# Kernel optimization log

Measured on AMD Instinct MI355X. Metric: run time of the kernel, lower is better.

The kernel has to match this reference:

```python
import jax, jax.numpy as jnp
import numpy as np

FILTER_K = 100  # filter_K from __init__
NUM_CLASSES = 1000


def setup_inputs() -> dict:
    key = jax.random.key(0)
    ks = jax.random.split(key, 7)
    B, Din, D, C, N = 256, 2048, 512, NUM_CLASSES, 50000
    x = jax.random.normal(ks[0], (B, Din), jnp.float32)
    Wf = jax.random.normal(ks[1], (Din, D), jnp.float32) * 0.02
    Wc = jax.random.normal(ks[2], (C, D), jnp.float32) * 0.05
    bc = jax.random.normal(ks[3], (C,), jnp.float32) * 0.01
    supports_in = jax.random.normal(ks[4], (N, D), jnp.float32)
    ent_in = jax.random.uniform(ks[5], (N,), jnp.float32)
    labels_idx = jax.random.randint(ks[6], (N,), 0, C)
    return {"x": x, "Wf": Wf, "Wc": Wc, "bc": bc,
            "supports_in": supports_in, "ent_in": ent_in, "labels_idx": labels_idx}


def _softmax_entropy(logits):
    # -(softmax * log_softmax).sum(1), computed stably in one pass
    logp = jax.nn.log_softmax(logits, axis=1)
    return -(jnp.exp(logp) * logp).sum(axis=1)


def reference(x, Wf, Wc, bc, supports_in, ent_in, labels_idx):
    C = Wc.shape[0]
    z = x @ Wf                    # featurizer: [B, D]
    p = z @ Wc.T + bc             # classifier logits: [B, C]
    yhat = jax.nn.one_hot(jnp.argmax(p, axis=1), C, dtype=z.dtype)
    ent_new = _softmax_entropy(p)
    labels_in = jax.nn.one_hot(labels_idx, C, dtype=z.dtype)

    # grow support memory
    supports = jnp.concatenate([supports_in, z], axis=0)   # [M, D]
    labels = jnp.concatenate([labels_in, yhat], axis=0)    # [M, C]
    ent = jnp.concatenate([ent_in, ent_new], axis=0)       # [M]

    # select_supports: per-class keep FILTER_K lowest-entropy entries.
    # Torch gathers a variable-size subset; equivalent fixed-shape form is a
    # boolean mask (non-selected rows contribute zero to the weights matmul).
    y = jnp.argmax(labels, axis=1)
    M = ent.shape[0]
    order = jnp.lexsort((ent, y))            # sort by class, then entropy
    y_sorted = y[order]
    # rank of each entry within its class segment
    rank = jnp.arange(M) - jnp.searchsorted(y_sorted, y_sorted, side='left')
    mask = jnp.zeros((M,), bool).at[order].set(rank < FILTER_K)
    maskf = mask.astype(z.dtype)

    # normalize supports row-wise (F.normalize, eps=1e-12), then masked matmul
    s_norm = supports / jnp.maximum(
        jnp.linalg.norm(supports, axis=1, keepdims=True), 1e-12)
    weights = (s_norm * maskf[:, None]).T @ (labels * maskf[:, None])  # [D, C]
    weights = weights / jnp.maximum(
        jnp.linalg.norm(weights, axis=0, keepdims=True), 1e-12)
    return z @ weights            # [B, C]
```

## Files before the change

kernel.cpp:

```cpp
#include <hip/hip_runtime.h>
#include <hip/hip_bf16.h>
#include <math.h>

#define BB   256
#define DIN  2048
#define DD   512
#define CC   1000
#define NN   50000
#define MM   (NN + BB)
#define FILTER_K 100
#define SLOT 512

#define SK1  32
#define SKP  8

#define Z_OFF     0
#define CNT_OFF   (Z_OFF + BB*DD)
#define ENTS_OFF  (CNT_OFF + 1024)
#define IDXS_OFF  (ENTS_OFF + CC*SLOT)
#define WN_OFF    (IDXS_OFF + CC*SLOT)
#define ZP_OFF    (WN_OFF + CC*DD)
#define PP_OFF    (ZP_OFF + SK1*BB*DD)
#define OP_OFF    (PP_OFF + SKP*BB*CC)

__global__ __launch_bounds__(256, 2) void gemm_ab_part(
    const float* __restrict__ A, const float* __restrict__ B,
    float* __restrict__ Cp) {
  __shared__ float As[16][68];
  __shared__ float Bs[16][132];
  const int tid = threadIdx.x;
  const int m0 = blockIdx.y * 64;
  const int n0 = blockIdx.x * 128;
  const int k0 = blockIdx.z * 64;
  const int ar = tid >> 2, ac = (tid & 3) * 4;
  const int br = tid >> 4, bcn = (tid & 15) * 8;
  const int tm = (tid >> 4) * 4, tn = (tid & 15) * 4;
  float acc[4][8] = {};
  float4 av  = *(const float4*)&A[(size_t)(m0 + ar) * DIN + k0 + ac];
  float4 bv0 = *(const float4*)&B[(size_t)(k0 + br) * DD + n0 + bcn];
  float4 bv1 = *(const float4*)&B[(size_t)(k0 + br) * DD + n0 + bcn + 4];
  for (int kk = 0; kk < 64; kk += 16) {
    __syncthreads();
    As[ac + 0][ar] = av.x; As[ac + 1][ar] = av.y;
    As[ac + 2][ar] = av.z; As[ac + 3][ar] = av.w;
    *(float4*)&Bs[br][bcn] = bv0;
    *(float4*)&Bs[br][bcn + 4] = bv1;
    __syncthreads();
    if (kk + 16 < 64) {
      av  = *(const float4*)&A[(size_t)(m0 + ar) * DIN + k0 + kk + 16 + ac];
      bv0 = *(const float4*)&B[(size_t)(k0 + kk + 16 + br) * DD + n0 + bcn];
      bv1 = *(const float4*)&B[(size_t)(k0 + kk + 16 + br) * DD + n0 + bcn + 4];
    }
#pragma unroll
    for (int q = 0; q < 16; ++q) {
      float4 a  = *(const float4*)&As[q][tm];
      float4 b0 = *(const float4*)&Bs[q][tn];
      float4 b1 = *(const float4*)&Bs[q][tn + 64];
      float aa[4] = {a.x, a.y, a.z, a.w};
      float bb[8] = {b0.x, b0.y, b0.z, b0.w, b1.x, b1.y, b1.z, b1.w};
#pragma unroll
      for (int i = 0; i < 4; ++i)
#pragma unroll
        for (int j = 0; j < 8; ++j) acc[i][j] += aa[i] * bb[j];
    }
  }
  float* Cb = Cp + (size_t)blockIdx.z * BB * DD;
#pragma unroll
  for (int i = 0; i < 4; ++i) {
    *(float4*)&Cb[(size_t)(m0 + tm + i) * DD + n0 + tn] =
        make_float4(acc[i][0], acc[i][1], acc[i][2], acc[i][3]);
    *(float4*)&Cb[(size_t)(m0 + tm + i) * DD + n0 + 64 + tn] =
        make_float4(acc[i][4], acc[i][5], acc[i][6], acc[i][7]);
  }
}

__global__ __launch_bounds__(256, 2) void gemm_abt_part(
    const float* __restrict__ A, const float* __restrict__ Bm,
    float* __restrict__ Cp) {
  __shared__ float As[16][68];
  __shared__ float Bs[16][68];
  const int tid = threadIdx.x;
  const int m0 = blockIdx.y * 64;
  const int n0 = blockIdx.x * 64;
  const int k0 = blockIdx.z * 64;
  const int ar = tid >> 2, ac = (tid & 3) * 4;
  const int tm = (tid >> 4) * 4, tn = (tid & 15) * 4;
  float acc[4][4] = {};
  float4 av = *(const float4*)&A[(size_t)(m0 + ar) * DD + k0 + ac];
  float4 bv = make_float4(0.f, 0.f, 0.f, 0.f);
  if (n0 + ar < CC) bv = *(const float4*)&Bm[(size_t)(n0 + ar) * DD + k0 + ac];
  for (int kk = 0; kk < 64; kk += 16) {
    __syncthreads();
    As[ac + 0][ar] = av.x; As[ac + 1][ar] = av.y;
    As[ac + 2][ar] = av.z; As[ac + 3][ar] = av.w;
    Bs[ac + 0][ar] = bv.x; Bs[ac + 1][ar] = bv.y;
    Bs[ac + 2][ar] = bv.z; Bs[ac + 3][ar] = bv.w;
    __syncthreads();
    if (kk + 16 < 64) {
      av = *(const float4*)&A[(size_t)(m0 + ar) * DD + k0 + kk + 16 + ac];
      if (n0 + ar < CC)
        bv = *(const float4*)&Bm[(size_t)(n0 + ar) * DD + k0 + kk + 16 + ac];
    }
#pragma unroll
    for (int q = 0; q < 16; ++q) {
      float4 a = *(const float4*)&As[q][tm];
      float4 b = *(const float4*)&Bs[q][tn];
      float aa[4] = {a.x, a.y, a.z, a.w};
      float bb[4] = {b.x, b.y, b.z, b.w};
#pragma unroll
      for (int i = 0; i < 4; ++i)
#pragma unroll
        for (int j = 0; j < 4; ++j) acc[i][j] += aa[i] * bb[j];
    }
  }
  float* Cb = Cp + (size_t)blockIdx.z * BB * CC;
#pragma unroll
  for (int i = 0; i < 4; ++i) {
    int n = n0 + tn;
    if (n + 3 < CC) {
      *(float4*)&Cb[(size_t)(m0 + tm + i) * CC + n] =
          make_float4(acc[i][0], acc[i][1], acc[i][2], acc[i][3]);
    } else {
#pragma unroll
      for (int j = 0; j < 4; ++j)
        if (n + j < CC) Cb[(size_t)(m0 + tm + i) * CC + n + j] = acc[i][j];
    }
  }
}

template <int S>
__global__ __launch_bounds__(256) void reduce_part(
    const float* __restrict__ part, float* __restrict__ out, int n4) {
  int i = blockIdx.x * 256 + threadIdx.x;
  if (i >= n4) return;
  const float4* p4 = (const float4*)part;
  float4 a = p4[i];
#pragma unroll
  for (int s = 1; s < S; ++s) {
    float4 b = p4[(size_t)s * n4 + i];
    a.x += b.x; a.y += b.y; a.z += b.z; a.w += b.w;
  }
  ((float4*)out)[i] = a;
}

__global__ void scatter_old(const int* __restrict__ labels_idx,
                            const float* __restrict__ ent_in,
                            int* __restrict__ cnt,
                            float* __restrict__ ent_s, int* __restrict__ idx_s) {
  int m = blockIdx.x * blockDim.x + threadIdx.x;
  if (m >= NN) return;
  int c = labels_idx[m];
  int pos = atomicAdd(&cnt[c], 1);
  if (pos < SLOT) {
    ent_s[(size_t)c * SLOT + pos] = ent_in[m];
    idx_s[(size_t)c * SLOT + pos] = m;
  }
}

__global__ __launch_bounds__(256) void rowstats(
    const float* __restrict__ ppart, const float* __restrict__ bc,
    int* __restrict__ cnt, float* __restrict__ ent_s,
    int* __restrict__ idx_s) {
  const int b = blockIdx.x, tid = threadIdx.x;
  const int lane = tid & 63, wid = tid >> 6;
  float r[4];
  float mv = -INFINITY; int mi = 0x7fffffff;
#pragma unroll
  for (int i = 0; i < 4; ++i) {
    int c = tid + 256 * i;
    if (c < CC) {
      float v = bc[c];
#pragma unroll
      for (int s = 0; s < SKP; ++s)
        v += ppart[(size_t)s * BB * CC + (size_t)b * CC + c];
      r[i] = v;
    } else r[i] = -INFINITY;
    if (r[i] > mv) { mv = r[i]; mi = c; }
  }
#pragma unroll
  for (int o = 32; o > 0; o >>= 1) {
    float ov = __shfl_down(mv, o, 64);
    int oi = __shfl_down(mi, o, 64);
    if (ov > mv || (ov == mv && oi < mi)) { mv = ov; mi = oi; }
  }
  __shared__ float smv[4]; __shared__ int smi[4];
  __shared__ float ssm[4], tsm[4];
  if (lane == 0) { smv[wid] = mv; smi[wid] = mi; }
  __syncthreads();
  if (tid == 0) {
#pragma unroll
    for (int w = 1; w < 4; ++w)
      if (smv[w] > smv[0] || (smv[w] == smv[0] && smi[w] < smi[0])) {
        smv[0] = smv[w]; smi[0] = smi[w];
      }
  }
  __syncthreads();
  const float m = smv[0]; const int am = smi[0];
  float s = 0.f, t = 0.f;
#pragma unroll
  for (int i = 0; i < 4; ++i) {
    if (tid + 256 * i < CC) {
      float u = r[i] - m;
      float e = expf(u);
      s += e; t += u * e;
    }
  }
#pragma unroll
  for (int o = 32; o > 0; o >>= 1) {
    s += __shfl_down(s, o, 64);
    t += __shfl_down(t, o, 64);
  }
  if (lane == 0) { ssm[wid] = s; tsm[wid] = t; }
  __syncthreads();
  if (tid == 0) {
    float S = ssm[0] + ssm[1] + ssm[2] + ssm[3];
    float T = tsm[0] + tsm[1] + tsm[2] + tsm[3];
    float ent = logf(S) - T / S;
    int pos = atomicAdd(&cnt[am], 1);
    if (pos < SLOT) {
      ent_s[(size_t)am * SLOT + pos] = ent;
      idx_s[(size_t)am * SLOT + pos] = NN + b;
    }
  }
}

__global__ __launch_bounds__(256) void class_weights(
    const float* __restrict__ supports_in, const float* __restrict__ z,
    const float* __restrict__ ent_s, const int* __restrict__ idx_s,
    const int* __restrict__ cnt, float* __restrict__ wn) {
  const int c = blockIdx.x, tid = threadIdx.x;
  const int lane = tid & 63, wid = tid >> 6;
  int n = cnt[c]; if (n > SLOT) n = SLOT;

  __shared__ int sel[SLOT];
  __shared__ float se[SLOT];
  __shared__ int si[SLOT];
  int seln;
  if (n <= FILTER_K) {
    seln = n;
    for (int i = tid; i < n; i += 256) sel[i] = idx_s[(size_t)c * SLOT + i];
  } else {
    for (int i = tid; i < SLOT; i += 256) {
      if (i < n) { se[i] = ent_s[(size_t)c * SLOT + i]; si[i] = idx_s[(size_t)c * SLOT + i]; }
      else       { se[i] = INFINITY;                     si[i] = 0x7fffffff; }
    }
    __syncthreads();
    for (int k = 2; k <= SLOT; k <<= 1)
      for (int j = k >> 1; j > 0; j >>= 1) {
        for (int i = tid; i < SLOT; i += 256) {
          int ixj = i ^ j;
          if (ixj > i) {
            bool up = ((i & k) == 0);
            float e1 = se[i], e2 = se[ixj];
            int i1 = si[i], i2 = si[ixj];
            bool gt = (e1 > e2) || (e1 == e2 && i1 > i2);
            if (gt == up) { se[i] = e2; se[ixj] = e1; si[i] = i2; si[ixj] = i1; }
          }
        }
        __syncthreads();
      }
    seln = FILTER_K;
    for (int i = tid; i < FILTER_K; i += 256) sel[i] = si[i];
  }
  __syncthreads();

  float4 a0 = make_float4(0.f, 0.f, 0.f, 0.f), a1 = a0;
  const int npair = seln >> 1;
  for (int t = wid; t < npair; t += 4) {
    int r0 = sel[2 * t], r1 = sel[2 * t + 1];
    const float4* p0 = (const float4*)((r0 < NN)
        ? supports_in + (size_t)r0 * DD : z + (size_t)(r0 - NN) * DD);
    const float4* p1 = (const float4*)((r1 < NN)
        ? supports_in + (size_t)r1 * DD : z + (size_t)(r1 - NN) * DD);
    float4 u0 = p0[lane * 2], u1 = p0[lane * 2 + 1];
    float4 w0 = p1[lane * 2], w1 = p1[lane * 2 + 1];
    float s0 = u0.x * u0.x + u0.y * u0.y + u0.z * u0.z + u0.w * u0.w
             + u1.x * u1.x + u1.y * u1.y + u1.z * u1.z + u1.w * u1.w;
    float s1 = w0.x * w0.x + w0.y * w0.y + w0.z * w0.z + w0.w * w0.w
             + w1.x * w1.x + w1.y * w1.y + w1.z * w1.z + w1.w * w1.w;
#pragma unroll
    for (int o = 1; o < 64; o <<= 1) {
      s0 += __shfl_xor(s0, o, 64);
      s1 += __shfl_xor(s1, o, 64);
    }
    float c0 = 1.0f / fmaxf(sqrtf(s0), 1e-12f);
    float c1 = 1.0f / fmaxf(sqrtf(s1), 1e-12f);
    a0.x += u0.x * c0 + w0.x * c1; a0.y += u0.y * c0 + w0.y * c1;
    a0.z += u0.z * c0 + w0.z * c1; a0.w += u0.w * c0 + w0.w * c1;
    a1.x += u1.x * c0 + w1.x * c1; a1.y += u1.y * c0 + w1.y * c1;
    a1.z += u1.z * c0 + w1.z * c1; a1.w += u1.w * c0 + w1.w * c1;
  }
  if ((seln & 1) && wid == (npair & 3)) {
    int r0 = sel[seln - 1];
    const float4* p0 = (const float4*)((r0 < NN)
        ? supports_in + (size_t)r0 * DD : z + (size_t)(r0 - NN) * DD);
    float4 u0 = p0[lane * 2], u1 = p0[lane * 2 + 1];
    float s0 = u0.x * u0.x + u0.y * u0.y + u0.z * u0.z + u0.w * u0.w
             + u1.x * u1.x + u1.y * u1.y + u1.z * u1.z + u1.w * u1.w;
#pragma unroll
    for (int o = 1; o < 64; o <<= 1) s0 += __shfl_xor(s0, o, 64);
    float c0 = 1.0f / fmaxf(sqrtf(s0), 1e-12f);
    a0.x += u0.x * c0; a0.y += u0.y * c0; a0.z += u0.z * c0; a0.w += u0.w * c0;
    a1.x += u1.x * c0; a1.y += u1.y * c0; a1.z += u1.z * c0; a1.w += u1.w * c0;
  }

  __shared__ float part[4][DD];
  *(float4*)&part[wid][lane * 8] = a0;
  *(float4*)&part[wid][lane * 8 + 4] = a1;
  __syncthreads();
  const int d = tid * 2;
  float wx = part[0][d] + part[1][d] + part[2][d] + part[3][d];
  float wy = part[0][d + 1] + part[1][d + 1] + part[2][d + 1] + part[3][d + 1];
  float ss = wx * wx + wy * wy;
#pragma unroll
  for (int o = 1; o < 64; o <<= 1) ss += __shfl_xor(ss, o, 64);
  __shared__ float tot[4];
  if (lane == 0) tot[wid] = ss;
  __syncthreads();
  float S = tot[0] + tot[1] + tot[2] + tot[3];
  float sc = 1.0f / fmaxf(sqrtf(S), 1e-12f);
  ((float2*)(wn + (size_t)c * DD))[tid] = make_float2(wx * sc, wy * sc);
}

extern "C" void kernel_launch(void* const* d_in, const int* in_sizes, int n_in,
                              void* d_out, int out_size, void* d_ws, size_t ws_size,
                              hipStream_t stream) {
  (void)in_sizes; (void)n_in; (void)out_size; (void)ws_size;
  const float* x           = (const float*)d_in[0];
  const float* Wf          = (const float*)d_in[1];
  const float* Wc          = (const float*)d_in[2];
  const float* bc          = (const float*)d_in[3];
  const float* supports_in = (const float*)d_in[4];
  const float* ent_in      = (const float*)d_in[5];
  const int*   labels_idx  = (const int*)d_in[6];
  float* out = (float*)d_out;

  float* W = (float*)d_ws;
  float* z     = W + Z_OFF;
  int*   cnt   = (int*)(W + CNT_OFF);
  float* ent_s = W + ENTS_OFF;
  int*   idx_s = (int*)(W + IDXS_OFF);
  float* wn    = W + WN_OFF;
  float* zpart = W + ZP_OFF;
  float* ppart = W + PP_OFF;
  float* opart = W + OP_OFF;

  hipMemsetAsync(cnt, 0, 1024 * sizeof(int), stream);

  scatter_old<<<(NN + 255) / 256, 256, 0, stream>>>(
      labels_idx, ent_in, cnt, ent_s, idx_s);

  gemm_ab_part<<<dim3(DD / 128, BB / 64, SK1), 256, 0, stream>>>(x, Wf, zpart);
  reduce_part<SK1><<<(BB * DD / 4 + 255) / 256, 256, 0, stream>>>(
      zpart, z, BB * DD / 4);

  gemm_abt_part<<<dim3((CC + 63) / 64, BB / 64, SKP), 256, 0, stream>>>(
      z, Wc, ppart);
  rowstats<<<BB, 256, 0, stream>>>(ppart, bc, cnt, ent_s, idx_s);

  class_weights<<<CC, 256, 0, stream>>>(supports_in, z, ent_s, idx_s, cnt, wn);

  gemm_abt_part<<<dim3((CC + 63) / 64, BB / 64, SKP), 256, 0, stream>>>(
      z, wn, opart);
  reduce_part<SKP><<<(BB * CC / 4 + 255) / 256, 256, 0, stream>>>(
      opart, out, BB * CC / 4);
}
```

Before: 225.9 us.

## Fuse scatter into first GEMM, batch support loads, replace split-K output GEMM

The label scatter is folded into the first GEMM launch as extra blocks past index 512, which removes one kernel launch and lets the scatter run alongside the GEMM. In class_weights, each wavefront now loads four support rows at once, padding the selection list to a multiple of 16 so more memory requests are in flight. The final z·wn product drops split-K and its reduction kernel in favour of a single full-K GEMM with 32x64 tiles. That removes the partial-sum buffer traffic and one launch, but each block now runs a longer serial K loop.

```diff
diff --git a/kernel.cpp b/kernel.cpp
--- a/kernel.cpp
+++ b/kernel.cpp
@@ -21,17 +21,31 @@
 #define WN_OFF    (IDXS_OFF + CC*SLOT)
 #define ZP_OFF    (WN_OFF + CC*DD)
 #define PP_OFF    (ZP_OFF + SK1*BB*DD)
-#define OP_OFF    (PP_OFF + SKP*BB*CC)
-
-__global__ __launch_bounds__(256, 2) void gemm_ab_part(
+
+__global__ __launch_bounds__(256, 2) void fused_scatter_gemm_ab(
     const float* __restrict__ A, const float* __restrict__ B,
-    float* __restrict__ Cp) {
+    float* __restrict__ Cp,
+    const int* __restrict__ labels_idx, const float* __restrict__ ent_in,
+    int* __restrict__ cnt, float* __restrict__ ent_s,
+    int* __restrict__ idx_s) {
   __shared__ float As[16][68];
   __shared__ float Bs[16][132];
-  const int tid = threadIdx.x;
-  const int m0 = blockIdx.y * 64;
-  const int n0 = blockIdx.x * 128;
-  const int k0 = blockIdx.z * 64;
+  const int gbid = blockIdx.x, tid = threadIdx.x;
+  if (gbid >= 512) {
+    int m = (gbid - 512) * 256 + tid;
+    if (m < NN) {
+      int c = labels_idx[m];
+      int pos = atomicAdd(&cnt[c], 1);
+      if (pos < SLOT) {
+        ent_s[(size_t)c * SLOT + pos] = ent_in[m];
+        idx_s[(size_t)c * SLOT + pos] = m;
+      }
+    }
+    return;
+  }
+  const int m0 = ((gbid >> 2) & 3) * 64;
+  const int n0 = (gbid & 3) * 128;
+  const int k0 = (gbid >> 4) * 64;
   const int ar = tid >> 2, ac = (tid & 3) * 4;
   const int br = tid >> 4, bcn = (tid & 15) * 8;
   const int tm = (tid >> 4) * 4, tn = (tid & 15) * 4;
@@ -64,7 +78,7 @@
         for (int j = 0; j < 8; ++j) acc[i][j] += aa[i] * bb[j];
     }
   }
-  float* Cb = Cp + (size_t)blockIdx.z * BB * DD;
+  float* Cb = Cp + (size_t)(gbid >> 4) * BB * DD;
 #pragma unroll
   for (int i = 0; i < 4; ++i) {
     *(float4*)&Cb[(size_t)(m0 + tm + i) * DD + n0 + tn] =
@@ -72,6 +86,21 @@
     *(float4*)&Cb[(size_t)(m0 + tm + i) * DD + n0 + 64 + tn] =
         make_float4(acc[i][4], acc[i][5], acc[i][6], acc[i][7]);
   }
+}
+
+template <int S>
+__global__ __launch_bounds__(256) void reduce_part(
+    const float* __restrict__ part, float* __restrict__ out, int n4) {
+  int i = blockIdx.x * 256 + threadIdx.x;
+  if (i >= n4) return;
+  const float4* p4 = (const float4*)part;
+  float4 a = p4[i];
+#pragma unroll
+  for (int s = 1; s < S; ++s) {
+    float4 b = p4[(size_t)s * n4 + i];
+    a.x += b.x; a.y += b.y; a.z += b.z; a.w += b.w;
+  }
+  ((float4*)out)[i] = a;
 }
 
 __global__ __launch_bounds__(256, 2) void gemm_abt_part(
@@ -128,35 +157,6 @@
   }
 }
 
-template <int S>
-__global__ __launch_bounds__(256) void reduce_part(
-    const float* __restrict__ part, float* __restrict__ out, int n4) {
-  int i = blockIdx.x * 256 + threadIdx.x;
-  if (i >= n4) return;
-  const float4* p4 = (const float4*)part;
-  float4 a = p4[i];
-#pragma unroll
-  for (int s = 1; s < S; ++s) {
-    float4 b = p4[(size_t)s * n4 + i];
-    a.x += b.x; a.y += b.y; a.z += b.z; a.w += b.w;
-  }
-  ((float4*)out)[i] = a;
-}
-
-__global__ void scatter_old(const int* __restrict__ labels_idx,
-                            const float* __restrict__ ent_in,
-                            int* __restrict__ cnt,
-                            float* __restrict__ ent_s, int* __restrict__ idx_s) {
-  int m = blockIdx.x * blockDim.x + threadIdx.x;
-  if (m >= NN) return;
-  int c = labels_idx[m];
-  int pos = atomicAdd(&cnt[c], 1);
-  if (pos < SLOT) {
-    ent_s[(size_t)c * SLOT + pos] = ent_in[m];
-    idx_s[(size_t)c * SLOT + pos] = m;
-  }
-}
-
 __global__ __launch_bounds__(256) void rowstats(
     const float* __restrict__ ppart, const float* __restrict__ bc,
     int* __restrict__ cnt, float* __restrict__ ent_s,
@@ -263,45 +263,39 @@
     for (int i = tid; i < FILTER_K; i += 256) sel[i] = si[i];
   }
   __syncthreads();
+  const int seln_pad = (seln + 15) & ~15;
+  if (seln > 0)
+    for (int i = seln + tid; i < seln_pad; i += 256) sel[i] = sel[0];
+  __syncthreads();
 
   float4 a0 = make_float4(0.f, 0.f, 0.f, 0.f), a1 = a0;
-  const int npair = seln >> 1;
-  for (int t = wid; t < npair; t += 4) {
-    int r0 = sel[2 * t], r1 = sel[2 * t + 1];
-    const float4* p0 = (const float4*)((r0 < NN)
-        ? supports_in + (size_t)r0 * DD : z + (size_t)(r0 - NN) * DD);
-    const float4* p1 = (const float4*)((r1 < NN)
-        ? supports_in + (size_t)r1 * DD : z + (size_t)(r1 - NN) * DD);
-    float4 u0 = p0[lane * 2], u1 = p0[lane * 2 + 1];
-    float4 w0 = p1[lane * 2], w1 = p1[lane * 2 + 1];
-    float s0 = u0.x * u0.x + u0.y * u0.y + u0.z * u0.z + u0.w * u0.w
-             + u1.x * u1.x + u1.y * u1.y + u1.z * u1.z + u1.w * u1.w;
-    float s1 = w0.x * w0.x + w0.y * w0.y + w0.z * w0.z + w0.w * w0.w
-             + w1.x * w1.x + w1.y * w1.y + w1.z * w1.z + w1.w * w1.w;
+  for (int t = wid * 4; t < seln_pad; t += 16) {
+    float4 u0[4], u1[4]; float s[4];
+#pragma unroll
+    for (int j = 0; j < 4; ++j) {
+      int r = sel[t + j];
+      const float4* p4 = (const float4*)((r < NN)
+          ? supports_in + (size_t)r * DD : z + (size_t)(r - NN) * DD);
+      u0[j] = p4[lane * 2]; u1[j] = p4[lane * 2 + 1];
+    }
+#pragma unroll
+    for (int j = 0; j < 4; ++j)
+      s[j] = u0[j].x * u0[j].x + u0[j].y * u0[j].y + u0[j].z * u0[j].z
+           + u0[j].w * u0[j].w + u1[j].x * u1[j].x + u1[j].y * u1[j].y
+           + u1[j].z * u1[j].z + u1[j].w * u1[j].w;
 #pragma unroll
     for (int o = 1; o < 64; o <<= 1) {
-      s0 += __shfl_xor(s0, o, 64);
-      s1 += __shfl_xor(s1, o, 64);
-    }
-    float c0 = 1.0f / fmaxf(sqrtf(s0), 1e-12f);
-    float c1 = 1.0f / fmaxf(sqrtf(s1), 1e-12f);
-    a0.x += u0.x * c0 + w0.x * c1; a0.y += u0.y * c0 + w0.y * c1;
-    a0.z += u0.z * c0 + w0.z * c1; a0.w += u0.w * c0 + w0.w * c1;
-    a1.x += u1.x * c0 + w1.x * c1; a1.y += u1.y * c0 + w1.y * c1;
-    a1.z += u1.z * c0 + w1.z * c1; a1.w += u1.w * c0 + w1.w * c1;
-  }
-  if ((seln & 1) && wid == (npair & 3)) {
-    int r0 = sel[seln - 1];
-    const float4* p0 = (const float4*)((r0 < NN)
-        ? supports_in + (size_t)r0 * DD : z + (size_t)(r0 - NN) * DD);
-    float4 u0 = p0[lane * 2], u1 = p0[lane * 2 + 1];
-    float s0 = u0.x * u0.x + u0.y * u0.y + u0.z * u0.z + u0.w * u0.w
-             + u1.x * u1.x + u1.y * u1.y + u1.z * u1.z + u1.w * u1.w;
-#pragma unroll
-    for (int o = 1; o < 64; o <<= 1) s0 += __shfl_xor(s0, o, 64);
-    float c0 = 1.0f / fmaxf(sqrtf(s0), 1e-12f);
-    a0.x += u0.x * c0; a0.y += u0.y * c0; a0.z += u0.z * c0; a0.w += u0.w * c0;
-    a1.x += u1.x * c0; a1.y += u1.y * c0; a1.z += u1.z * c0; a1.w += u1.w * c0;
+#pragma unroll
+      for (int j = 0; j < 4; ++j) s[j] += __shfl_xor(s[j], o, 64);
+    }
+#pragma unroll
+    for (int j = 0; j < 4; ++j) {
+      float sc = (t + j < seln) ? 1.0f / fmaxf(sqrtf(s[j]), 1e-12f) : 0.f;
+      a0.x += u0[j].x * sc; a0.y += u0[j].y * sc;
+      a0.z += u0[j].z * sc; a0.w += u0[j].w * sc;
+      a1.x += u1[j].x * sc; a1.y += u1[j].y * sc;
+      a1.z += u1[j].z * sc; a1.w += u1[j].w * sc;
+    }
   }
 
   __shared__ float part[4][DD];
@@ -320,6 +314,58 @@
   float S = tot[0] + tot[1] + tot[2] + tot[3];
   float sc = 1.0f / fmaxf(sqrtf(S), 1e-12f);
   ((float2*)(wn + (size_t)c * DD))[tid] = make_float2(wx * sc, wy * sc);
+}
+
+__global__ __launch_bounds__(256, 2) void gemm_out(
+    const float* __restrict__ A, const float* __restrict__ Bm,
+    float* __restrict__ C) {
+  __shared__ float As[16][36];
+  __shared__ float Bs[16][68];
+  const int tid = threadIdx.x;
+  const int m0 = blockIdx.y * 32;
+  const int n0 = blockIdx.x * 64;
+  const int ar = tid >> 3, ac = (tid & 7) * 2;
+  const int br = tid >> 2, bc = (tid & 3) * 4;
+  const int tm = (tid >> 4) * 2, tn = (tid & 15) * 4;
+  float acc[2][4] = {};
+  float2 av = *(const float2*)&A[(size_t)(m0 + ar) * DD + ac];
+  float4 bv = make_float4(0.f, 0.f, 0.f, 0.f);
+  if (n0 + br < CC) bv = *(const float4*)&Bm[(size_t)(n0 + br) * DD + bc];
+  for (int k0 = 0; k0 < DD; k0 += 16) {
+    __syncthreads();
+    As[ac + 0][ar] = av.x; As[ac + 1][ar] = av.y;
+    Bs[bc + 0][br] = bv.x; Bs[bc + 1][br] = bv.y;
+    Bs[bc + 2][br] = bv.z; Bs[bc + 3][br] = bv.w;
+    __syncthreads();
+    if (k0 + 16 < DD) {
+      av = *(const float2*)&A[(size_t)(m0 + ar) * DD + k0 + 16 + ac];
+      if (n0 + br < CC)
+        bv = *(const float4*)&Bm[(size_t)(n0 + br) * DD + k0 + 16 + bc];
+    }
+#pragma unroll
+    for (int q = 0; q < 16; ++q) {
+      float2 a = *(const float2*)&As[q][tm];
+      float4 b = *(const float4*)&Bs[q][tn];
+      float aa[2] = {a.x, a.y};
+      float bb[4] = {b.x, b.y, b.z, b.w};
+#pragma unroll
+      for (int i = 0; i < 2; ++i)
+#pragma unroll
+        for (int j = 0; j < 4; ++j) acc[i][j] += aa[i] * bb[j];
+    }
+  }
+#pragma unroll
+  for (int i = 0; i < 2; ++i) {
+    int n = n0 + tn;
+    if (n + 3 < CC) {
+      *(float4*)&C[(size_t)(m0 + tm + i) * CC + n] =
+          make_float4(acc[i][0], acc[i][1], acc[i][2], acc[i][3]);
+    } else {
+#pragma unroll
+      for (int j = 0; j < 4; ++j)
+        if (n + j < CC) C[(size_t)(m0 + tm + i) * CC + n + j] = acc[i][j];
+    }
+  }
 }
 
 extern "C" void kernel_launch(void* const* d_in, const int* in_sizes, int n_in,
@@ -343,25 +389,15 @@
   float* wn    = W + WN_OFF;
   float* zpart = W + ZP_OFF;
   float* ppart = W + PP_OFF;
-  float* opart = W + OP_OFF;
 
   hipMemsetAsync(cnt, 0, 1024 * sizeof(int), stream);
-
-  scatter_old<<<(NN + 255) / 256, 256, 0, stream>>>(
-      labels_idx, ent_in, cnt, ent_s, idx_s);
-
-  gemm_ab_part<<<dim3(DD / 128, BB / 64, SK1), 256, 0, stream>>>(x, Wf, zpart);
+  fused_scatter_gemm_ab<<<512 + (NN + 255) / 256, 256, 0, stream>>>(
+      x, Wf, zpart, labels_idx, ent_in, cnt, ent_s, idx_s);
   reduce_part<SK1><<<(BB * DD / 4 + 255) / 256, 256, 0, stream>>>(
       zpart, z, BB * DD / 4);
-
   gemm_abt_part<<<dim3((CC + 63) / 64, BB / 64, SKP), 256, 0, stream>>>(
       z, Wc, ppart);
   rowstats<<<BB, 256, 0, stream>>>(ppart, bc, cnt, ent_s, idx_s);
-
   class_weights<<<CC, 256, 0, stream>>>(supports_in, z, ent_s, idx_s, cnt, wn);
-
-  gemm_abt_part<<<dim3((CC + 63) / 64, BB / 64, SKP), 256, 0, stream>>>(
-      z, wn, opart);
-  reduce_part<SKP><<<(BB * CC / 4 + 255) / 256, 256, 0, stream>>>(
-      opart, out, BB * CC / 4);
-}
+  gemm_out<<<dim3((CC + 63) / 64, BB / 32), 256, 0, stream>>>(z, wn, out);
+}
```

After: 228.3 us. Within noise of the previous version (+1.1%).
